# Performance work log

Hardware: AMD Instinct MI355X
Metric: run time of the kernel (lower is better)

## Reference

```python
import jax, jax.numpy as jnp
import numpy as np

G, P, D, K = 64, 1024, 64, 6  # graphs, nodes/graph, features, knn k
N = G * P


def _lin_init(k, shape):
    s = 1.0 / np.sqrt(shape[0])
    return jax.random.uniform(k, shape, minval=-s, maxval=s, dtype=jnp.float32)


def setup_inputs() -> dict:
    key = jax.random.key(0)
    ks = jax.random.split(key, 16)
    return {
        "x": jax.random.normal(ks[0], (N, D), jnp.float32),
        "batchidxs": jnp.repeat(jnp.arange(G, dtype=jnp.int32), P),
        "pre_W1": _lin_init(ks[1], (D, D)),
        "pre_b1": _lin_init(ks[2], (D,)),
        "pre_a1": jnp.full((D,), 0.25, jnp.float32),
        "pre_W2": _lin_init(ks[3], (D, D)),
        "pre_b2": _lin_init(ks[4], (D,)),
        "pre_a2": jnp.full((D,), 0.25, jnp.float32),
        "bn_gamma": jnp.ones((D,), jnp.float32),
        "bn_beta": jnp.zeros((D,), jnp.float32),
        "act_a": jnp.full((D,), 0.25, jnp.float32),
        "conv_W": jax.random.normal(ks[5], (4, D, D), jnp.float32) / np.sqrt(D),
        "conv_b": jnp.zeros((4, D), jnp.float32),
        "ffn_W1": _lin_init(ks[6], (5 * D, 5 * D)),
        "ffn_b1": _lin_init(ks[7], (5 * D,)),
        "ffn_W2": _lin_init(ks[8], (5 * D, 1)),
        "ffn_b2": _lin_init(ks[9], (1,)),
    }


def _prelu(x, a):
    return jnp.where(x >= 0, x, a * x)


def _knn_edges(x):
    """knn_graph with k=K per graph (equal-sized graphs). Returns (src, dst) global idx."""
    xg = x.reshape(G, P, D)

    def knn_one(pts):  # [P, D] -> [P, K] local neighbor idx
        sq = jnp.sum(pts * pts, axis=-1)
        d2 = sq[:, None] + sq[None, :] - 2.0 * (pts @ pts.T)
        d2 = d2 + jnp.eye(P, dtype=d2.dtype) * 1e10  # exclude self-loop
        _, idx = jax.lax.top_k(-d2, K)
        return idx

    nbr = jax.vmap(knn_one)(xg)  # [G, P, K]
    offs = (jnp.arange(G, dtype=nbr.dtype) * P)[:, None, None]
    src = (nbr + offs).reshape(-1)  # source (neighbor) nodes x_j
    dst = jnp.broadcast_to(jnp.arange(P, dtype=nbr.dtype)[None, :, None] + offs,
                           (G, P, K)).reshape(-1)  # target (query) nodes
    return src, dst


def reference(x, batchidxs, pre_W1, pre_b1, pre_a1, pre_W2, pre_b2, pre_a2,
              bn_gamma, bn_beta, act_a, conv_W, conv_b,
              ffn_W1, ffn_b1, ffn_W2, ffn_b2):
    src, dst = _knn_edges(x)

    # pre_nn: Linear -> PReLU -> Linear -> PReLU -> BatchNorm (training stats)
    h = _prelu(x @ pre_W1 + pre_b1, pre_a1)
    h = _prelu(h @ pre_W2 + pre_b2, pre_a2)
    mu = jnp.mean(h, axis=0)
    var = jnp.var(h, axis=0)
    h = (h - mu) * jax.lax.rsqrt(var + 1e-5) * bn_gamma + bn_beta

    xs = [h]
    for i in range(4):
        msg = h[src] @ conv_W[i] + conv_b[i]            # gather + transform [E, D]
        aggr = jax.ops.segment_sum(msg, dst, num_segments=N)  # scatter-add
        h = _prelu(aggr + h, act_a)                     # shared PReLU act
        xs.append(h)

    hc = jnp.concatenate(xs, axis=-1)                   # JumpingKnowledge 'cat' [N, 5D]
    pooled = jax.ops.segment_sum(hc, batchidxs, num_segments=G)  # global_add_pool [G, 5D]

    # hlv_dnn FFN(5D -> 1): Linear -> LeakyReLU -> Linear
    z = pooled @ ffn_W1 + ffn_b1
    z = jnp.where(z >= 0, z, 0.01 * z)
    return z @ ffn_W2 + ffn_b2
```

## Files before the change

### kernel.cpp

```cpp
#include <hip/hip_runtime.h>


typedef float4 f4;
typedef unsigned short ushort;
typedef unsigned int uint;
typedef _Float16 f16;
typedef _Float16 f16x8 __attribute__((ext_vector_type(8)));
typedef float f32x16 __attribute__((ext_vector_type(16)));

#define FMA16(sv, wv) do { \
  a0.x += (sv).x*(wv).x; a0.y += (sv).x*(wv).y; a0.z += (sv).x*(wv).z; a0.w += (sv).x*(wv).w; \
  a1.x += (sv).y*(wv).x; a1.y += (sv).y*(wv).y; a1.z += (sv).y*(wv).z; a1.w += (sv).y*(wv).w; \
  a2.x += (sv).z*(wv).x; a2.y += (sv).z*(wv).y; a2.z += (sv).z*(wv).z; a2.w += (sv).z*(wv).w; \
  a3.x += (sv).w*(wv).x; a3.y += (sv).w*(wv).y; a3.z += (sv).w*(wv).z; a3.w += (sv).w*(wv).w; \
} while (0)

union HU { f16 h; ushort u; };
__device__ __forceinline__ ushort f2h_u(float f) { HU x; x.h = (f16)f; return x.u; }
__device__ __forceinline__ f16 u2h(ushort u) { HU x; x.u = u; return x.h; }

__device__ __forceinline__ uint med3u(uint a, uint b, uint c) {
  uint d;
  asm("v_med3_u32 %0, %1, %2, %3" : "=v"(d) : "v"(a), "v"(b), "v"(c));
  return d;
}

#define INSM(x) do { \
  m5 = med3u((x), m4, m5); \
  m4 = med3u((x), m3, m4); \
  m3 = med3u((x), m2, m3); \
  m2 = med3u((x), m1, m2); \
  m1 = med3u((x), m0, m1); \
  m0 = max(m0, (x)); \
} while (0)

__global__ __launch_bounds__(256, 4) void kknn(const ushort* __restrict__ xf16,
                                               const uint* __restrict__ sq2,
                                               int* __restrict__ nbr) {
  __shared__ uint skey[4][32][6];
  const int tid = threadIdx.x;
  const int lane = tid & 63;
  const int w = tid >> 6;
  const int q = lane & 31;
  const int h = lane >> 5;
  const int g = blockIdx.x >> 5;
  const int qtile = blockIdx.x & 31;
  const int gbase = g << 10;
  const int qloc = qtile * 32 + q;
  const int qglob = gbase + qloc;

  f16x8 Q0, Q1, Q2, Q3;
  {
    const ushort* qp = xf16 + (size_t)qglob * 64 + 8 * h;
    Q0 = *(const f16x8*)(qp);       Q1 = *(const f16x8*)(qp + 16);
    Q2 = *(const f16x8*)(qp + 32);  Q3 = *(const f16x8*)(qp + 48);
  }
  f16x8 Bsq = {(f16)0, (f16)0, (f16)0, (f16)0, (f16)0, (f16)0, (f16)0, (f16)0};
  if (h == 0) { Bsq[0] = (f16)1.0f; Bsq[1] = (f16)1.0f; }

  uint m0 = 0, m1 = 0, m2 = 0, m3 = 0, m4 = 0, m5 = 0;

  for (int cc = 0; cc < 8; ++cc) {
    const int cg = w * 8 + cc;
    const int cb = gbase + cg * 32;
    const ushort* cp = xf16 + (size_t)(cb + q) * 64 + 8 * h;
    f16x8 A0 = *(const f16x8*)(cp);       f16x8 A1 = *(const f16x8*)(cp + 16);
    f16x8 A2 = *(const f16x8*)(cp + 32);  f16x8 A3 = *(const f16x8*)(cp + 48);
    uint sv = sq2[cb + q];
    f16x8 Asq = {(f16)0, (f16)0, (f16)0, (f16)0, (f16)0, (f16)0, (f16)0, (f16)0};
    if (h == 0) { Asq[0] = u2h((ushort)(sv & 0xffffu)); Asq[1] = u2h((ushort)(sv >> 16)); }

    f32x16 acc = {1536.f,1536.f,1536.f,1536.f,1536.f,1536.f,1536.f,1536.f,
                  1536.f,1536.f,1536.f,1536.f,1536.f,1536.f,1536.f,1536.f};
    acc = __builtin_amdgcn_mfma_f32_32x32x16_f16(A0, Q0, acc, 0, 0, 0);
    acc = __builtin_amdgcn_mfma_f32_32x32x16_f16(A1, Q1, acc, 0, 0, 0);
    acc = __builtin_amdgcn_mfma_f32_32x32x16_f16(A2, Q2, acc, 0, 0, 0);
    acc = __builtin_amdgcn_mfma_f32_32x32x16_f16(A3, Q3, acc, 0, 0, 0);
    acc = __builtin_amdgcn_mfma_f32_32x32x16_f16(Asq, Bsq, acc, 0, 0, 0);

    const int cl0 = cg * 32 + 4 * h;
    const uint kb = (uint)(1023 - cl0);
    if (cg == qtile) {
#pragma unroll
      for (int r = 0; r < 16; ++r) {
        const int pat = (r & 3) + 8 * (r >> 2);
        uint u = __float_as_uint(acc[r]);
        uint key = (((u << 9) & 0xFFFFFC00u) | kb) - (uint)pat;
        if (cl0 + pat == qloc) key = 0u;
        INSM(key);
      }
    } else {
#pragma unroll
      for (int r = 0; r < 16; ++r) {
        const int pat = (r & 3) + 8 * (r >> 2);
        uint u = __float_as_uint(acc[r]);
        uint key = (((u << 9) & 0xFFFFFC00u) | kb) - (uint)pat;
        INSM(key);
      }
    }
  }

  {
    uint p0 = (uint)__shfl_xor((int)m0, 32, 64);
    uint p1 = (uint)__shfl_xor((int)m1, 32, 64);
    uint p2 = (uint)__shfl_xor((int)m2, 32, 64);
    uint p3 = (uint)__shfl_xor((int)m3, 32, 64);
    uint p4 = (uint)__shfl_xor((int)m4, 32, 64);
    uint p5 = (uint)__shfl_xor((int)m5, 32, 64);
    INSM(p0); INSM(p1); INSM(p2); INSM(p3); INSM(p4); INSM(p5);
  }
  if (h == 0) {
    skey[w][q][0] = m0; skey[w][q][1] = m1; skey[w][q][2] = m2;
    skey[w][q][3] = m3; skey[w][q][4] = m4; skey[w][q][5] = m5;
  }
  __syncthreads();

  if (tid < 32) {
    uint m0 = skey[0][tid][0], m1 = skey[0][tid][1], m2 = skey[0][tid][2];
    uint m3 = skey[0][tid][3], m4 = skey[0][tid][4], m5 = skey[0][tid][5];
#pragma unroll
    for (int ww = 1; ww < 4; ++ww)
#pragma unroll
      for (int k = 0; k < 6; ++k)
        INSM(skey[ww][tid][k]);
    const int ob = (gbase + qtile * 32 + tid) * 6;
    nbr[ob + 0] = gbase + 1023 - (int)(m0 & 1023u);
    nbr[ob + 1] = gbase + 1023 - (int)(m1 & 1023u);
    nbr[ob + 2] = gbase + 1023 - (int)(m2 & 1023u);
    nbr[ob + 3] = gbase + 1023 - (int)(m3 & 1023u);
    nbr[ob + 4] = gbase + 1023 - (int)(m4 & 1023u);
    nbr[ob + 5] = gbase + 1023 - (int)(m5 & 1023u);
  }
}

__global__ __launch_bounds__(256) void kpre(const float* __restrict__ x,
    const float* __restrict__ W1, const float* __restrict__ b1, const float* __restrict__ p1,
    const float* __restrict__ W2, const float* __restrict__ b2, const float* __restrict__ p2,
    float* __restrict__ hpre, float* __restrict__ gsumg, float* __restrict__ gsq,
    ushort* __restrict__ xf16, uint* __restrict__ sq2) {
  __shared__ float xT[64][68];
  __shared__ float yT[64][68];
  __shared__ float W1l[64][64];
  __shared__ float W2l[64][64];
  __shared__ float bb1[64], aa1[64], bb2[64], aa2[64];
  __shared__ float ls[64], lq[64];
  __shared__ float ls2[64][4];
  const int tid = threadIdx.x;
  const int base = blockIdx.x * 64;
  const int g = base >> 10;
#pragma unroll
  for (int k = 0; k < 16; ++k) {
    int idx = tid + 256 * k;
    W1l[idx >> 6][idx & 63] = W1[idx];
    W2l[idx >> 6][idx & 63] = W2[idx];
  }
  if (tid < 64) {
    bb1[tid] = b1[tid]; aa1[tid] = p1[tid]; bb2[tid] = b2[tid]; aa2[tid] = p2[tid];
    ls[tid] = 0.f; lq[tid] = 0.f;
  }
  const int il = tid >> 2, qq = tid & 3;
  {
    const f4* src = (const f4*)(x + (size_t)(base + il) * 64) + qq * 4;
    float ssq = 0.f;
#pragma unroll
    for (int m = 0; m < 4; ++m) {
      f4 v = src[m];
      int d0 = qq * 16 + m * 4;
      xT[d0+0][il] = v.x; xT[d0+1][il] = v.y; xT[d0+2][il] = v.z; xT[d0+3][il] = v.w;
      ushort4 o4;
      o4.x = f2h_u(v.x); o4.y = f2h_u(v.y); o4.z = f2h_u(v.z); o4.w = f2h_u(v.w);
      *(ushort4*)(xf16 + (size_t)(base + il) * 64 + d0) = o4;
      ssq += v.x*v.x + v.y*v.y + v.z*v.z + v.w*v.w;
    }
    ls2[il][qq] = ssq;
  }
  __syncthreads();
  if (tid < 64) {
    float s = ls2[tid][0] + ls2[tid][1] + ls2[tid][2] + ls2[tid][3];
    float mm = -0.5f * s;
    ushort h1 = f2h_u(mm);
    HU t; t.u = h1;
    ushort h2 = f2h_u(mm - (float)t.h);
    sq2[base + tid] = (uint)h1 | ((uint)h2 << 16);
  }
  const int ti = tid & 15, to = tid >> 4;
  f4 a0 = {0.f,0.f,0.f,0.f}, a1 = a0, a2 = a0, a3 = a0;
#pragma unroll 16
  for (int d = 0; d < 64; ++d) {
    f4 sv = *(const f4*)&xT[d][4*ti];
    f4 wv = *(const f4*)&W1l[d][4*to];
    FMA16(sv, wv);
  }
#define EPI1(AR, r) { \
    const int row = 4*ti + (r); float v; \
    v = AR.x + bb1[4*to+0]; v = v >= 0.f ? v : aa1[4*to+0]*v; yT[4*to+0][row] = v; \
    v = AR.y + bb1[4*to+1]; v = v >= 0.f ? v : aa1[4*to+1]*v; yT[4*to+1][row] = v; \
    v = AR.z + bb1[4*to+2]; v = v >= 0.f ? v : aa1[4*to+2]*v; yT[4*to+2][row] = v; \
    v = AR.w + bb1[4*to+3]; v = v >= 0.f ? v : aa1[4*to+3]*v; yT[4*to+3][row] = v; }
  EPI1(a0, 0) EPI1(a1, 1) EPI1(a2, 2) EPI1(a3, 3)
#undef EPI1
  __syncthreads();
  a0.x=a0.y=a0.z=a0.w=0.f; a1=a0; a2=a0; a3=a0;
#pragma unroll 16
  for (int d = 0; d < 64; ++d) {
    f4 sv = *(const f4*)&yT[d][4*ti];
    f4 wv = *(const f4*)&W2l[d][4*to];
    FMA16(sv, wv);
  }
  float fs0=0.f,fs1=0.f,fs2=0.f,fs3=0.f, fq0=0.f,fq1=0.f,fq2=0.f,fq3=0.f;
#define EPI2(AR, r) { \
    const int i = base + 4*ti + (r); f4 ov; float v; \
    v = AR.x + bb2[4*to+0]; ov.x = v >= 0.f ? v : aa2[4*to+0]*v; \
    v = AR.y + bb2[4*to+1]; ov.y = v >= 0.f ? v : aa2[4*to+1]*v; \
    v = AR.z + bb2[4*to+2]; ov.z = v >= 0.f ? v : aa2[4*to+2]*v; \
    v = AR.w + bb2[4*to+3]; ov.w = v >= 0.f ? v : aa2[4*to+3]*v; \
    fs0 += ov.x; fq0 += ov.x*ov.x; fs1 += ov.y; fq1 += ov.y*ov.y; \
    fs2 += ov.z; fq2 += ov.z*ov.z; fs3 += ov.w; fq3 += ov.w*ov.w; \
    *((f4*)(hpre + (size_t)i * 64) + to) = ov; }
  EPI2(a0, 0) EPI2(a1, 1) EPI2(a2, 2) EPI2(a3, 3)
#undef EPI2
  atomicAdd(&ls[4*to+0], fs0); atomicAdd(&lq[4*to+0], fq0);
  atomicAdd(&ls[4*to+1], fs1); atomicAdd(&lq[4*to+1], fq1);
  atomicAdd(&ls[4*to+2], fs2); atomicAdd(&lq[4*to+2], fq2);
  atomicAdd(&ls[4*to+3], fs3); atomicAdd(&lq[4*to+3], fq3);
  __syncthreads();
  if (tid < 64) {
    atomicAdd(&gsumg[g * 64 + tid], ls[tid]);
    atomicAdd(&gsq[tid], lq[tid]);
  }
}

__global__ void kfin(const float* __restrict__ gsumg, const float* __restrict__ gsq,
                     const float* __restrict__ gamma, const float* __restrict__ beta,
                     float* __restrict__ scale, float* __restrict__ shift,
                     float* __restrict__ pooled) {
  const int g = blockIdx.x, f = threadIdx.x;
  float s = 0.f;
  for (int g2 = 0; g2 < 64; ++g2) s += gsumg[g2 * 64 + f];
  float mu = s * (1.f / 65536.f);
  float var = gsq[f] * (1.f / 65536.f) - mu * mu;
  float sc = gamma[f] * rsqrtf(var + 1e-5f);
  float sh = beta[f] - mu * sc;
  pooled[g * 320 + f] = sc * gsumg[g * 64 + f] + 1024.f * sh;
  if (g == 0) { scale[f] = sc; shift[f] = sh; }
}

template <int BN>
__global__ __launch_bounds__(256) void kconv(const float* __restrict__ hIn,
    float* __restrict__ hOut, const int* __restrict__ nbr,
    const float* __restrict__ W, const float* __restrict__ bias,
    const float* __restrict__ act, const float* __restrict__ scale,
    const float* __restrict__ shift, float* __restrict__ pooled, int stageoff) {
  __shared__ float sT[64][68];
  __shared__ float Wl[64][64];
  __shared__ float bb[64], aa[64], pool[64];
  __shared__ float scl[64], shl[64];
  const int tid = threadIdx.x;
  const int base = blockIdx.x * 64;
  const int g = base >> 10;
#pragma unroll
  for (int k = 0; k < 16; ++k) { int idx = tid + 256 * k; Wl[idx >> 6][idx & 63] = W[idx]; }
  if (tid < 64) {
    bb[tid] = bias[tid]; aa[tid] = act[tid]; pool[tid] = 0.f;
    if (BN) { scl[tid] = scale[tid]; shl[tid] = shift[tid]; }
  }

  const int il = tid >> 2, qq = tid & 3;
  {
    f4 acc0 = {0.f,0.f,0.f,0.f}, acc1 = acc0, acc2 = acc0, acc3 = acc0;
    const int i = base + il;
#pragma unroll
    for (int k = 0; k < 6; ++k) {
      int j = nbr[i * 6 + k];
      const f4* hj = (const f4*)(hIn + (size_t)j * 64) + qq * 4;
      f4 v0 = hj[0], v1 = hj[1], v2 = hj[2], v3 = hj[3];
      acc0.x += v0.x; acc0.y += v0.y; acc0.z += v0.z; acc0.w += v0.w;
      acc1.x += v1.x; acc1.y += v1.y; acc1.z += v1.z; acc1.w += v1.w;
      acc2.x += v2.x; acc2.y += v2.y; acc2.z += v2.z; acc2.w += v2.w;
      acc3.x += v3.x; acc3.y += v3.y; acc3.z += v3.z; acc3.w += v3.w;
    }
    const int d0 = qq * 16;
    sT[d0+ 0][il]=acc0.x; sT[d0+ 1][il]=acc0.y; sT[d0+ 2][il]=acc0.z; sT[d0+ 3][il]=acc0.w;
    sT[d0+ 4][il]=acc1.x; sT[d0+ 5][il]=acc1.y; sT[d0+ 6][il]=acc1.z; sT[d0+ 7][il]=acc1.w;
    sT[d0+ 8][il]=acc2.x; sT[d0+ 9][il]=acc2.y; sT[d0+10][il]=acc2.z; sT[d0+11][il]=acc2.w;
    sT[d0+12][il]=acc3.x; sT[d0+13][il]=acc3.y; sT[d0+14][il]=acc3.z; sT[d0+15][il]=acc3.w;
  }
  __syncthreads();

  const int ti = tid & 15, to = tid >> 4;
  f4 a0 = {0.f,0.f,0.f,0.f}, a1 = a0, a2 = a0, a3 = a0;
  if (BN) {
#pragma unroll 16
    for (int d = 0; d < 64; ++d) {
      const float scd = scl[d], shd6 = 6.f * shl[d];
      f4 sv = *(const f4*)&sT[d][4*ti];
      sv.x = sv.x * scd + shd6; sv.y = sv.y * scd + shd6;
      sv.z = sv.z * scd + shd6; sv.w = sv.w * scd + shd6;
      f4 wv = *(const f4*)&Wl[d][4*to];
      FMA16(sv, wv);
    }
  } else {
#pragma unroll 16
    for (int d = 0; d < 64; ++d) {
      f4 sv = *(const f4*)&sT[d][4*ti];
      f4 wv = *(const f4*)&Wl[d][4*to];
      FMA16(sv, wv);
    }
  }

  const float bs0 = 6.f*bb[4*to+0], bs1 = 6.f*bb[4*to+1], bs2 = 6.f*bb[4*to+2], bs3 = 6.f*bb[4*to+3];
  const float av0 = aa[4*to+0], av1 = aa[4*to+1], av2 = aa[4*to+2], av3 = aa[4*to+3];
  const float rs0 = BN ? scl[4*to+0] : 1.f, rs1 = BN ? scl[4*to+1] : 1.f;
  const float rs2 = BN ? scl[4*to+2] : 1.f, rs3 = BN ? scl[4*to+3] : 1.f;
  const float rh0 = BN ? shl[4*to+0] : 0.f, rh1 = BN ? shl[4*to+1] : 0.f;
  const float rh2 = BN ? shl[4*to+2] : 0.f, rh3 = BN ? shl[4*to+3] : 0.f;
  float p0 = 0.f, pp1 = 0.f, pp2 = 0.f, pp3 = 0.f;
#define CEPI(AR, r) { \
    const int i = base + 4*ti + (r); \
    f4 res = *((const f4*)(hIn + (size_t)i * 64) + to); \
    f4 ov; float v; \
    v = AR.x + bs0 + res.x*rs0 + rh0; v = v >= 0.f ? v : av0 * v; ov.x = v; p0  += v; \
    v = AR.y + bs1 + res.y*rs1 + rh1; v = v >= 0.f ? v : av1 * v; ov.y = v; pp1 += v; \
    v = AR.z + bs2 + res.z*rs2 + rh2; v = v >= 0.f ? v : av2 * v; ov.z = v; pp2 += v; \
    v = AR.w + bs3 + res.w*rs3 + rh3; v = v >= 0.f ? v : av3 * v; ov.w = v; pp3 += v; \
    *((f4*)(hOut + (size_t)i * 64) + to) = ov; }
  CEPI(a0, 0) CEPI(a1, 1) CEPI(a2, 2) CEPI(a3, 3)
#undef CEPI
  atomicAdd(&pool[4*to+0], p0);
  atomicAdd(&pool[4*to+1], pp1);
  atomicAdd(&pool[4*to+2], pp2);
  atomicAdd(&pool[4*to+3], pp3);
  __syncthreads();
  if (tid < 64) atomicAdd(&pooled[g * 320 + stageoff + tid], pool[tid]);
}

__global__ __launch_bounds__(256) void kffn(const float* __restrict__ pooled,
    const float* __restrict__ W1, const float* __restrict__ b1,
    const float* __restrict__ W2, const float* __restrict__ b2,
    float* __restrict__ out) {
  __shared__ float pg[320];
  __shared__ float z1[320];
  __shared__ float red[4];
  const int g = blockIdx.x, tid = threadIdx.x;
  for (int i = tid; i < 320; i += 256) pg[i] = pooled[g * 320 + i];
  __syncthreads();
  for (int o = tid; o < 320; o += 256) {
    float acc = b1[o];
    for (int d = 0; d < 320; ++d) acc += pg[d] * W1[d * 320 + o];
    z1[o] = acc >= 0.f ? acc : 0.01f * acc;
  }
  __syncthreads();
  float p = 0.f;
  for (int o = tid; o < 320; o += 256) p += z1[o] * W2[o];
#pragma unroll
  for (int m = 32; m; m >>= 1) p += __shfl_xor(p, m, 64);
  if ((tid & 63) == 0) red[tid >> 6] = p;
  __syncthreads();
  if (tid == 0) out[g] = red[0] + red[1] + red[2] + red[3] + b2[0];
}

extern "C" void kernel_launch(void* const* d_in, const int* in_sizes, int n_in,
                              void* d_out, int out_size, void* d_ws, size_t ws_size,
                              hipStream_t stream) {
  const float* x        = (const float*)d_in[0];
  const float* pre_W1   = (const float*)d_in[2];
  const float* pre_b1   = (const float*)d_in[3];
  const float* pre_a1   = (const float*)d_in[4];
  const float* pre_W2   = (const float*)d_in[5];
  const float* pre_b2   = (const float*)d_in[6];
  const float* pre_a2   = (const float*)d_in[7];
  const float* bn_gamma = (const float*)d_in[8];
  const float* bn_beta  = (const float*)d_in[9];
  const float* act_a    = (const float*)d_in[10];
  const float* conv_W   = (const float*)d_in[11];
  const float* conv_b   = (const float*)d_in[12];
  const float* ffn_W1   = (const float*)d_in[13];
  const float* ffn_b1   = (const float*)d_in[14];
  const float* ffn_W2   = (const float*)d_in[15];
  const float* ffn_b2   = (const float*)d_in[16];
  float* out = (float*)d_out;

  float* ws = (float*)d_ws;
  float* hA = ws;
  float* hB = ws + 4194304;
  ushort* xf16 = (ushort*)hB;
  uint*   sq2  = (uint*)(hB + 2097152);
  int*   nbr   = (int*)(ws + 8388608);
  float* stats = ws + 8388608 + 393216;
  float* gsq    = stats;
  float* gsumg  = stats + 64;
  float* scale  = stats + 64 + 4096;
  float* shift  = stats + 64 + 4096 + 64;
  float* pooled = stats + 64 + 4096 + 128;

  hipMemsetAsync(stats, 0, (64 + 4096 + 128 + 64 * 320) * sizeof(float), stream);

  kpre  <<<1024, 256, 0, stream>>>(x, pre_W1, pre_b1, pre_a1, pre_W2, pre_b2, pre_a2,
                                   hA, gsumg, gsq, xf16, sq2);
  kknn  <<<2048, 256, 0, stream>>>(xf16, sq2, nbr);
  kfin  <<<64, 64, 0, stream>>>(gsumg, gsq, bn_gamma, bn_beta, scale, shift, pooled);
  kconv<1><<<1024, 256, 0, stream>>>(hA, hB, nbr, conv_W,         conv_b,       act_a, scale, shift, pooled, 64);
  kconv<0><<<1024, 256, 0, stream>>>(hB, hA, nbr, conv_W + 4096,  conv_b + 64,  act_a, scale, shift, pooled, 128);
  kconv<0><<<1024, 256, 0, stream>>>(hA, hB, nbr, conv_W + 8192,  conv_b + 128, act_a, scale, shift, pooled, 192);
  kconv<0><<<1024, 256, 0, stream>>>(hB, hA, nbr, conv_W + 12288, conv_b + 192, act_a, scale, shift, pooled, 256);
  kffn  <<<64, 256, 0, stream>>>(pooled, ffn_W1, ffn_b1, ffn_W2, ffn_b2, out);
}
```

Baseline: 300.9 us.

## Use fp16 MFMA for pre-MLP and conv layers with fp16 activations

```diff
diff --git a/kernel.cpp b/kernel.cpp
--- a/kernel.cpp
+++ b/kernel.cpp
@@ -8,12 +8,7 @@
 typedef _Float16 f16x8 __attribute__((ext_vector_type(8)));
 typedef float f32x16 __attribute__((ext_vector_type(16)));
 
-#define FMA16(sv, wv) do { \
-  a0.x += (sv).x*(wv).x; a0.y += (sv).x*(wv).y; a0.z += (sv).x*(wv).z; a0.w += (sv).x*(wv).w; \
-  a1.x += (sv).y*(wv).x; a1.y += (sv).y*(wv).y; a1.z += (sv).y*(wv).z; a1.w += (sv).y*(wv).w; \
-  a2.x += (sv).z*(wv).x; a2.y += (sv).z*(wv).y; a2.z += (sv).z*(wv).z; a2.w += (sv).z*(wv).w; \
-  a3.x += (sv).w*(wv).x; a3.y += (sv).w*(wv).y; a3.z += (sv).w*(wv).z; a3.w += (sv).w*(wv).w; \
-} while (0)
+#define Z16 {0.f,0.f,0.f,0.f,0.f,0.f,0.f,0.f,0.f,0.f,0.f,0.f,0.f,0.f,0.f,0.f}
 
 union HU { f16 h; ushort u; };
 __device__ __forceinline__ ushort f2h_u(float f) { HU x; x.h = (f16)f; return x.u; }
@@ -33,6 +28,17 @@
   m1 = med3u((x), m0, m1); \
   m0 = max(m0, (x)); \
 } while (0)
+
+__global__ void kwprep(const float* __restrict__ W1, const float* __restrict__ W2,
+                       const float* __restrict__ convW, ushort* __restrict__ wt) {
+  const int m = blockIdx.x;
+  const float* src = (m == 0) ? W1 : (m == 1) ? W2 : convW + (m - 2) * 4096;
+  ushort* dst = wt + m * 4096;
+  for (int i = threadIdx.x; i < 4096; i += 256) {
+    int k = i >> 6, n = i & 63;
+    dst[n * 64 + k] = f2h_u(src[i]);
+  }
+}
 
 __global__ __launch_bounds__(256, 4) void kknn(const ushort* __restrict__ xf16,
                                                const uint* __restrict__ sq2,
@@ -133,96 +139,105 @@
   }
 }
 
-__global__ __launch_bounds__(256) void kpre(const float* __restrict__ x,
-    const float* __restrict__ W1, const float* __restrict__ b1, const float* __restrict__ p1,
-    const float* __restrict__ W2, const float* __restrict__ b2, const float* __restrict__ p2,
-    float* __restrict__ hpre, float* __restrict__ gsumg, float* __restrict__ gsq,
+__global__ __launch_bounds__(256) void kpre(
+    const float* __restrict__ x, const ushort* __restrict__ w1t,
+    const float* __restrict__ b1, const float* __restrict__ p1,
+    const ushort* __restrict__ w2t, const float* __restrict__ b2,
+    const float* __restrict__ p2, ushort* __restrict__ hout,
+    float* __restrict__ gsumg, float* __restrict__ gsq,
     ushort* __restrict__ xf16, uint* __restrict__ sq2) {
-  __shared__ float xT[64][68];
-  __shared__ float yT[64][68];
-  __shared__ float W1l[64][64];
-  __shared__ float W2l[64][64];
-  __shared__ float bb1[64], aa1[64], bb2[64], aa2[64];
+  __shared__ ushort tile[4][32][72];
   __shared__ float ls[64], lq[64];
-  __shared__ float ls2[64][4];
-  const int tid = threadIdx.x;
-  const int base = blockIdx.x * 64;
-  const int g = base >> 10;
-#pragma unroll
-  for (int k = 0; k < 16; ++k) {
-    int idx = tid + 256 * k;
-    W1l[idx >> 6][idx & 63] = W1[idx];
-    W2l[idx >> 6][idx & 63] = W2[idx];
-  }
-  if (tid < 64) {
-    bb1[tid] = b1[tid]; aa1[tid] = p1[tid]; bb2[tid] = b2[tid]; aa2[tid] = p2[tid];
-    ls[tid] = 0.f; lq[tid] = 0.f;
-  }
-  const int il = tid >> 2, qq = tid & 3;
+  const int tid = threadIdx.x, lane = tid & 63, w = tid >> 6;
+  const int q = lane & 31, h = lane >> 5;
+  const int rbase = blockIdx.x * 128 + w * 32;
+  const int row = rbase + q;
+  const int g = blockIdx.x >> 3;
+  if (tid < 64) { ls[tid] = 0.f; lq[tid] = 0.f; }
+  __syncthreads();
+
+  f16x8 Ax[4]; float ssq = 0.f;
+  const float* xp = x + (size_t)row * 64 + 8 * h;
+  ushort* xo = xf16 + (size_t)row * 64 + 8 * h;
+#pragma unroll
+  for (int ks = 0; ks < 4; ++ks) {
+    f4 a = *(const f4*)(xp + 16 * ks);
+    f4 b = *(const f4*)(xp + 16 * ks + 4);
+    f16x8 f;
+    f[0] = (f16)a.x; f[1] = (f16)a.y; f[2] = (f16)a.z; f[3] = (f16)a.w;
+    f[4] = (f16)b.x; f[5] = (f16)b.y; f[6] = (f16)b.z; f[7] = (f16)b.w;
+    Ax[ks] = f;
+    *(f16x8*)(xo + 16 * ks) = f;
+    ssq += a.x*a.x + a.y*a.y + a.z*a.z + a.w*a.w + b.x*b.x + b.y*b.y + b.z*b.z + b.w*b.w;
+  }
+  ssq += __shfl_xor(ssq, 32, 64);
+  if (h == 0) {
+    float mm = -0.5f * ssq;
+    ushort u1 = f2h_u(mm); HU t1; t1.u = u1;
+    ushort u2 = f2h_u(mm - (float)t1.h);
+    sq2[row] = (uint)u1 | ((uint)u2 << 16);
+  }
+
+  f32x16 c0 = Z16, c1 = Z16;
+#pragma unroll
+  for (int ks = 0; ks < 4; ++ks) {
+    f16x8 B0 = *(const f16x8*)(w1t + q * 64 + 16 * ks + 8 * h);
+    f16x8 B1 = *(const f16x8*)(w1t + (q + 32) * 64 + 16 * ks + 8 * h);
+    c0 = __builtin_amdgcn_mfma_f32_32x32x16_f16(Ax[ks], B0, c0, 0, 0, 0);
+    c1 = __builtin_amdgcn_mfma_f32_32x32x16_f16(Ax[ks], B1, c1, 0, 0, 0);
+  }
   {
-    const f4* src = (const f4*)(x + (size_t)(base + il) * 64) + qq * 4;
-    float ssq = 0.f;
-#pragma unroll
-    for (int m = 0; m < 4; ++m) {
-      f4 v = src[m];
-      int d0 = qq * 16 + m * 4;
-      xT[d0+0][il] = v.x; xT[d0+1][il] = v.y; xT[d0+2][il] = v.z; xT[d0+3][il] = v.w;
-      ushort4 o4;
-      o4.x = f2h_u(v.x); o4.y = f2h_u(v.y); o4.z = f2h_u(v.z); o4.w = f2h_u(v.w);
-      *(ushort4*)(xf16 + (size_t)(base + il) * 64 + d0) = o4;
-      ssq += v.x*v.x + v.y*v.y + v.z*v.z + v.w*v.w;
-    }
-    ls2[il][qq] = ssq;
-  }
-  __syncthreads();
-  if (tid < 64) {
-    float s = ls2[tid][0] + ls2[tid][1] + ls2[tid][2] + ls2[tid][3];
-    float mm = -0.5f * s;
-    ushort h1 = f2h_u(mm);
-    HU t; t.u = h1;
-    ushort h2 = f2h_u(mm - (float)t.h);
-    sq2[base + tid] = (uint)h1 | ((uint)h2 << 16);
-  }
-  const int ti = tid & 15, to = tid >> 4;
-  f4 a0 = {0.f,0.f,0.f,0.f}, a1 = a0, a2 = a0, a3 = a0;
-#pragma unroll 16
-  for (int d = 0; d < 64; ++d) {
-    f4 sv = *(const f4*)&xT[d][4*ti];
-    f4 wv = *(const f4*)&W1l[d][4*to];
-    FMA16(sv, wv);
-  }
-#define EPI1(AR, r) { \
-    const int row = 4*ti + (r); float v; \
-    v = AR.x + bb1[4*to+0]; v = v >= 0.f ? v : aa1[4*to+0]*v; yT[4*to+0][row] = v; \
-    v = AR.y + bb1[4*to+1]; v = v >= 0.f ? v : aa1[4*to+1]*v; yT[4*to+1][row] = v; \
-    v = AR.z + bb1[4*to+2]; v = v >= 0.f ? v : aa1[4*to+2]*v; yT[4*to+2][row] = v; \
-    v = AR.w + bb1[4*to+3]; v = v >= 0.f ? v : aa1[4*to+3]*v; yT[4*to+3][row] = v; }
-  EPI1(a0, 0) EPI1(a1, 1) EPI1(a2, 2) EPI1(a3, 3)
-#undef EPI1
-  __syncthreads();
-  a0.x=a0.y=a0.z=a0.w=0.f; a1=a0; a2=a0; a3=a0;
-#pragma unroll 16
-  for (int d = 0; d < 64; ++d) {
-    f4 sv = *(const f4*)&yT[d][4*ti];
-    f4 wv = *(const f4*)&W2l[d][4*to];
-    FMA16(sv, wv);
-  }
-  float fs0=0.f,fs1=0.f,fs2=0.f,fs3=0.f, fq0=0.f,fq1=0.f,fq2=0.f,fq3=0.f;
-#define EPI2(AR, r) { \
-    const int i = base + 4*ti + (r); f4 ov; float v; \
-    v = AR.x + bb2[4*to+0]; ov.x = v >= 0.f ? v : aa2[4*to+0]*v; \
-    v = AR.y + bb2[4*to+1]; ov.y = v >= 0.f ? v : aa2[4*to+1]*v; \
-    v = AR.z + bb2[4*to+2]; ov.z = v >= 0.f ? v : aa2[4*to+2]*v; \
-    v = AR.w + bb2[4*to+3]; ov.w = v >= 0.f ? v : aa2[4*to+3]*v; \
-    fs0 += ov.x; fq0 += ov.x*ov.x; fs1 += ov.y; fq1 += ov.y*ov.y; \
-    fs2 += ov.z; fq2 += ov.z*ov.z; fs3 += ov.w; fq3 += ov.w*ov.w; \
-    *((f4*)(hpre + (size_t)i * 64) + to) = ov; }
-  EPI2(a0, 0) EPI2(a1, 1) EPI2(a2, 2) EPI2(a3, 3)
-#undef EPI2
-  atomicAdd(&ls[4*to+0], fs0); atomicAdd(&lq[4*to+0], fq0);
-  atomicAdd(&ls[4*to+1], fs1); atomicAdd(&lq[4*to+1], fq1);
-  atomicAdd(&ls[4*to+2], fs2); atomicAdd(&lq[4*to+2], fq2);
-  atomicAdd(&ls[4*to+3], fs3); atomicAdd(&lq[4*to+3], fq3);
+    const float bb0 = b1[q], aa0 = p1[q], bb1 = b1[q + 32], aa1 = p1[q + 32];
+#pragma unroll
+    for (int r = 0; r < 16; ++r) {
+      const int nd = (r & 3) + 8 * (r >> 2) + 4 * h;
+      float v0 = c0[r] + bb0; v0 = v0 >= 0.f ? v0 : aa0 * v0;
+      float v1 = c1[r] + bb1; v1 = v1 >= 0.f ? v1 : aa1 * v1;
+      tile[w][nd][q] = f2h_u(v0);
+      tile[w][nd][q + 32] = f2h_u(v1);
+    }
+  }
+  f16x8 Ah[4];
+#pragma unroll
+  for (int ks = 0; ks < 4; ++ks)
+    Ah[ks] = *(const f16x8*)&tile[w][q][16 * ks + 8 * h];
+
+  f32x16 d0 = Z16, d1 = Z16;
+#pragma unroll
+  for (int ks = 0; ks < 4; ++ks) {
+    f16x8 B0 = *(const f16x8*)(w2t + q * 64 + 16 * ks + 8 * h);
+    f16x8 B1 = *(const f16x8*)(w2t + (q + 32) * 64 + 16 * ks + 8 * h);
+    d0 = __builtin_amdgcn_mfma_f32_32x32x16_f16(Ah[ks], B0, d0, 0, 0, 0);
+    d1 = __builtin_amdgcn_mfma_f32_32x32x16_f16(Ah[ks], B1, d1, 0, 0, 0);
+  }
+  {
+    const float bb0 = b2[q], aa0 = p2[q], bb1 = b2[q + 32], aa1 = p2[q + 32];
+    float s0 = 0.f, q0 = 0.f, s1 = 0.f, q1 = 0.f;
+#pragma unroll
+    for (int r = 0; r < 16; ++r) {
+      const int nd = (r & 3) + 8 * (r >> 2) + 4 * h;
+      float v0 = d0[r] + bb0; v0 = v0 >= 0.f ? v0 : aa0 * v0;
+      float v1 = d1[r] + bb1; v1 = v1 >= 0.f ? v1 : aa1 * v1;
+      ushort u0 = f2h_u(v0), u1 = f2h_u(v1);
+      HU t0, t1; t0.u = u0; t1.u = u1;
+      float r0 = (float)t0.h, r1 = (float)t1.h;
+      s0 += r0; q0 += r0 * r0; s1 += r1; q1 += r1 * r1;
+      tile[w][nd][q] = u0;
+      tile[w][nd][q + 32] = u1;
+    }
+    s0 += __shfl_xor(s0, 32, 64); q0 += __shfl_xor(q0, 32, 64);
+    s1 += __shfl_xor(s1, 32, 64); q1 += __shfl_xor(q1, 32, 64);
+    if (h == 0) {
+      atomicAdd(&ls[q], s0); atomicAdd(&lq[q], q0);
+      atomicAdd(&ls[q + 32], s1); atomicAdd(&lq[q + 32], q1);
+    }
+  }
+  ushort* ho = hout + (size_t)row * 64 + 8 * h;
+#pragma unroll
+  for (int ks = 0; ks < 4; ++ks) {
+    f16x8 v = *(const f16x8*)&tile[w][q][16 * ks + 8 * h];
+    *(f16x8*)(ho + 16 * ks) = v;
+  }
   __syncthreads();
   if (tid < 64) {
     atomicAdd(&gsumg[g * 64 + tid], ls[tid]);
@@ -246,90 +261,113 @@
 }
 
 template <int BN>
-__global__ __launch_bounds__(256) void kconv(const float* __restrict__ hIn,
-    float* __restrict__ hOut, const int* __restrict__ nbr,
-    const float* __restrict__ W, const float* __restrict__ bias,
-    const float* __restrict__ act, const float* __restrict__ scale,
-    const float* __restrict__ shift, float* __restrict__ pooled, int stageoff) {
-  __shared__ float sT[64][68];
-  __shared__ float Wl[64][64];
-  __shared__ float bb[64], aa[64], pool[64];
-  __shared__ float scl[64], shl[64];
-  const int tid = threadIdx.x;
-  const int base = blockIdx.x * 64;
-  const int g = base >> 10;
-#pragma unroll
-  for (int k = 0; k < 16; ++k) { int idx = tid + 256 * k; Wl[idx >> 6][idx & 63] = W[idx]; }
-  if (tid < 64) {
-    bb[tid] = bias[tid]; aa[tid] = act[tid]; pool[tid] = 0.f;
-    if (BN) { scl[tid] = scale[tid]; shl[tid] = shift[tid]; }
-  }
-
-  const int il = tid >> 2, qq = tid & 3;
+__global__ __launch_bounds__(256) void kconv(
+    const ushort* __restrict__ hIn, ushort* __restrict__ hOut,
+    const int* __restrict__ nbr, const ushort* __restrict__ wt,
+    const float* __restrict__ bias, const float* __restrict__ act,
+    const float* __restrict__ scale, const float* __restrict__ shift,
+    float* __restrict__ pooled, int stageoff) {
+  __shared__ ushort tile[4][32][72];
+  __shared__ float pool[64];
+  const int tid = threadIdx.x, lane = tid & 63, w = tid >> 6;
+  const int q = lane & 31, h = lane >> 5;
+  const int nbase = blockIdx.x * 128 + w * 32;
+  const int node = nbase + q;
+  const int g = blockIdx.x >> 3;
+  if (tid < 64) pool[tid] = 0.f;
+  __syncthreads();
+
+  const int* np = nbr + (size_t)node * 6;
+  const int j0 = np[0], j1 = np[1], j2 = np[2], j3 = np[3], j4 = np[4], j5 = np[5];
+
+  f16x8 Af[4];
+#pragma unroll
+  for (int ks = 0; ks < 4; ++ks) {
+    const int off = 16 * ks + 8 * h;
+    float s0=0.f,s1=0.f,s2=0.f,s3=0.f,s4=0.f,s5=0.f,s6=0.f,s7=0.f;
+#define ACC6(J) { f16x8 v = *(const f16x8*)(hIn + (size_t)(J) * 64 + off); \
+    s0 += (float)v[0]; s1 += (float)v[1]; s2 += (float)v[2]; s3 += (float)v[3]; \
+    s4 += (float)v[4]; s5 += (float)v[5]; s6 += (float)v[6]; s7 += (float)v[7]; }
+    ACC6(j0) ACC6(j1) ACC6(j2) ACC6(j3) ACC6(j4) ACC6(j5)
+#undef ACC6
+    if (BN) {
+      f4 sa = *(const f4*)(scale + off), sb = *(const f4*)(scale + off + 4);
+      f4 ha = *(const f4*)(shift + off), hb = *(const f4*)(shift + off + 4);
+      s0 = s0*sa.x + 6.f*ha.x; s1 = s1*sa.y + 6.f*ha.y;
+      s2 = s2*sa.z + 6.f*ha.z; s3 = s3*sa.w + 6.f*ha.w;
+      s4 = s4*sb.x + 6.f*hb.x; s5 = s5*sb.y + 6.f*hb.y;
+      s6 = s6*sb.z + 6.f*hb.z; s7 = s7*sb.w + 6.f*hb.w;
+    }
+    f16x8 f;
+    f[0]=(f16)s0; f[1]=(f16)s1; f[2]=(f16)s2; f[3]=(f16)s3;
+    f[4]=(f16)s4; f[5]=(f16)s5; f[6]=(f16)s6; f[7]=(f16)s7;
+    Af[ks] = f;
+  }
+
+  f32x16 c0 = Z16, c1 = Z16;
+#pragma unroll
+  for (int ks = 0; ks < 4; ++ks) {
+    f16x8 B0 = *(const f16x8*)(wt + q * 64 + 16 * ks + 8 * h);
+    f16x8 B1 = *(const f16x8*)(wt + (q + 32) * 64 + 16 * ks + 8 * h);
+    c0 = __builtin_amdgcn_mfma_f32_32x32x16_f16(Af[ks], B0, c0, 0, 0, 0);
+    c1 = __builtin_amdgcn_mfma_f32_32x32x16_f16(Af[ks], B1, c1, 0, 0, 0);
+  }
   {
-    f4 acc0 = {0.f,0.f,0.f,0.f}, acc1 = acc0, acc2 = acc0, acc3 = acc0;
-    const int i = base + il;
-#pragma unroll
-    for (int k = 0; k < 6; ++k) {
-      int j = nbr[i * 6 + k];
-      const f4* hj = (const f4*)(hIn + (size_t)j * 64) + qq * 4;
-      f4 v0 = hj[0], v1 = hj[1], v2 = hj[2], v3 = hj[3];
-      acc0.x += v0.x; acc0.y += v0.y; acc0.z += v0.z; acc0.w += v0.w;
-      acc1.x += v1.x; acc1.y += v1.y; acc1.z += v1.z; acc1.w += v1.w;
-      acc2.x += v2.x; acc2.y += v2.y; acc2.z += v2.z; acc2.w += v2.w;
-      acc3.x += v3.x; acc3.y += v3.y; acc3.z += v3.z; acc3.w += v3.w;
-    }
-    const int d0 = qq * 16;
-    sT[d0+ 0][il]=acc0.x; sT[d0+ 1][il]=acc0.y; sT[d0+ 2][il]=acc0.z; sT[d0+ 3][il]=acc0.w;
-    sT[d0+ 4][il]=acc1.x; sT[d0+ 5][il]=acc1.y; sT[d0+ 6][il]=acc1.z; sT[d0+ 7][il]=acc1.w;
-    sT[d0+ 8][il]=acc2.x; sT[d0+ 9][il]=acc2.y; sT[d0+10][il]=acc2.z; sT[d0+11][il]=acc2.w;
-    sT[d0+12][il]=acc3.x; sT[d0+13][il]=acc3.y; sT[d0+14][il]=acc3.z; sT[d0+15][il]=acc3.w;
-  }
-  __syncthreads();
-
-  const int ti = tid & 15, to = tid >> 4;
-  f4 a0 = {0.f,0.f,0.f,0.f}, a1 = a0, a2 = a0, a3 = a0;
+    const float bb0 = 6.f * bias[q], bb1 = 6.f * bias[q + 32];
+#pragma unroll
+    for (int r = 0; r < 16; ++r) {
+      const int nd = (r & 3) + 8 * (r >> 2) + 4 * h;
+      tile[w][nd][q] = f2h_u(c0[r] + bb0);
+      tile[w][nd][q + 32] = f2h_u(c1[r] + bb1);
+    }
+  }
+
+  const int a = lane >> 3, b = lane & 7;
+  f4 aa0 = *(const f4*)(act + 8 * b), aa1 = *(const f4*)(act + 8 * b + 4);
+  f4 rs0, rs1, rh0, rh1;
   if (BN) {
-#pragma unroll 16
-    for (int d = 0; d < 64; ++d) {
-      const float scd = scl[d], shd6 = 6.f * shl[d];
-      f4 sv = *(const f4*)&sT[d][4*ti];
-      sv.x = sv.x * scd + shd6; sv.y = sv.y * scd + shd6;
-      sv.z = sv.z * scd + shd6; sv.w = sv.w * scd + shd6;
-      f4 wv = *(const f4*)&Wl[d][4*to];
-      FMA16(sv, wv);
-    }
-  } else {
-#pragma unroll 16
-    for (int d = 0; d < 64; ++d) {
-      f4 sv = *(const f4*)&sT[d][4*ti];
-      f4 wv = *(const f4*)&Wl[d][4*to];
-      FMA16(sv, wv);
-    }
-  }
-
-  const float bs0 = 6.f*bb[4*to+0], bs1 = 6.f*bb[4*to+1], bs2 = 6.f*bb[4*to+2], bs3 = 6.f*bb[4*to+3];
-  const float av0 = aa[4*to+0], av1 = aa[4*to+1], av2 = aa[4*to+2], av3 = aa[4*to+3];
-  const float rs0 = BN ? scl[4*to+0] : 1.f, rs1 = BN ? scl[4*to+1] : 1.f;
-  const float rs2 = BN ? scl[4*to+2] : 1.f, rs3 = BN ? scl[4*to+3] : 1.f;
-  const float rh0 = BN ? shl[4*to+0] : 0.f, rh1 = BN ? shl[4*to+1] : 0.f;
-  const float rh2 = BN ? shl[4*to+2] : 0.f, rh3 = BN ? shl[4*to+3] : 0.f;
-  float p0 = 0.f, pp1 = 0.f, pp2 = 0.f, pp3 = 0.f;
-#define CEPI(AR, r) { \
-    const int i = base + 4*ti + (r); \
-    f4 res = *((const f4*)(hIn + (size_t)i * 64) + to); \
-    f4 ov; float v; \
-    v = AR.x + bs0 + res.x*rs0 + rh0; v = v >= 0.f ? v : av0 * v; ov.x = v; p0  += v; \
-    v = AR.y + bs1 + res.y*rs1 + rh1; v = v >= 0.f ? v : av1 * v; ov.y = v; pp1 += v; \
-    v = AR.z + bs2 + res.z*rs2 + rh2; v = v >= 0.f ? v : av2 * v; ov.z = v; pp2 += v; \
-    v = AR.w + bs3 + res.w*rs3 + rh3; v = v >= 0.f ? v : av3 * v; ov.w = v; pp3 += v; \
-    *((f4*)(hOut + (size_t)i * 64) + to) = ov; }
-  CEPI(a0, 0) CEPI(a1, 1) CEPI(a2, 2) CEPI(a3, 3)
-#undef CEPI
-  atomicAdd(&pool[4*to+0], p0);
-  atomicAdd(&pool[4*to+1], pp1);
-  atomicAdd(&pool[4*to+2], pp2);
-  atomicAdd(&pool[4*to+3], pp3);
+    rs0 = *(const f4*)(scale + 8 * b); rs1 = *(const f4*)(scale + 8 * b + 4);
+    rh0 = *(const f4*)(shift + 8 * b); rh1 = *(const f4*)(shift + 8 * b + 4);
+  }
+  f4 ps0 = {0.f,0.f,0.f,0.f}, ps1 = ps0;
+#pragma unroll
+  for (int r = 0; r < 4; ++r) {
+    const int nd = 4 * a + r;
+    const size_t gn = (size_t)(nbase + nd) * 64 + 8 * b;
+    f16x8 z = *(const f16x8*)&tile[w][nd][8 * b];
+    f16x8 ro = *(const f16x8*)(hIn + gn);
+    float v0 = (float)z[0] + (BN ? rs0.x * (float)ro[0] + rh0.x : (float)ro[0]);
+    float v1 = (float)z[1] + (BN ? rs0.y * (float)ro[1] + rh0.y : (float)ro[1]);
+    float v2 = (float)z[2] + (BN ? rs0.z * (float)ro[2] + rh0.z : (float)ro[2]);
+    float v3 = (float)z[3] + (BN ? rs0.w * (float)ro[3] + rh0.w : (float)ro[3]);
+    float v4 = (float)z[4] + (BN ? rs1.x * (float)ro[4] + rh1.x : (float)ro[4]);
+    float v5 = (float)z[5] + (BN ? rs1.y * (float)ro[5] + rh1.y : (float)ro[5]);
+    float v6 = (float)z[6] + (BN ? rs1.z * (float)ro[6] + rh1.z : (float)ro[6]);
+    float v7 = (float)z[7] + (BN ? rs1.w * (float)ro[7] + rh1.w : (float)ro[7]);
+    v0 = v0 >= 0.f ? v0 : aa0.x * v0;  v1 = v1 >= 0.f ? v1 : aa0.y * v1;
+    v2 = v2 >= 0.f ? v2 : aa0.z * v2;  v3 = v3 >= 0.f ? v3 : aa0.w * v3;
+    v4 = v4 >= 0.f ? v4 : aa1.x * v4;  v5 = v5 >= 0.f ? v5 : aa1.y * v5;
+    v6 = v6 >= 0.f ? v6 : aa1.z * v6;  v7 = v7 >= 0.f ? v7 : aa1.w * v7;
+    ps0.x += v0; ps0.y += v1; ps0.z += v2; ps0.w += v3;
+    ps1.x += v4; ps1.y += v5; ps1.z += v6; ps1.w += v7;
+    f16x8 o;
+    o[0]=(f16)v0; o[1]=(f16)v1; o[2]=(f16)v2; o[3]=(f16)v3;
+    o[4]=(f16)v4; o[5]=(f16)v5; o[6]=(f16)v6; o[7]=(f16)v7;
+    *(f16x8*)(hOut + gn) = o;
+  }
+#pragma unroll
+  for (int m = 8; m <= 32; m <<= 1) {
+    ps0.x += __shfl_xor(ps0.x, m, 64); ps0.y += __shfl_xor(ps0.y, m, 64);
+    ps0.z += __shfl_xor(ps0.z, m, 64); ps0.w += __shfl_xor(ps0.w, m, 64);
+    ps1.x += __shfl_xor(ps1.x, m, 64); ps1.y += __shfl_xor(ps1.y, m, 64);
+    ps1.z += __shfl_xor(ps1.z, m, 64); ps1.w += __shfl_xor(ps1.w, m, 64);
+  }
+  if (a == 0) {
+    atomicAdd(&pool[8 * b + 0], ps0.x); atomicAdd(&pool[8 * b + 1], ps0.y);
+    atomicAdd(&pool[8 * b + 2], ps0.z); atomicAdd(&pool[8 * b + 3], ps0.w);
+    atomicAdd(&pool[8 * b + 4], ps1.x); atomicAdd(&pool[8 * b + 5], ps1.y);
+    atomicAdd(&pool[8 * b + 6], ps1.z); atomicAdd(&pool[8 * b + 7], ps1.w);
+  }
   __syncthreads();
   if (tid < 64) atomicAdd(&pooled[g * 320 + stageoff + tid], pool[tid]);
 }
@@ -380,13 +418,13 @@
   const float* ffn_b2   = (const float*)d_in[16];
   float* out = (float*)d_out;
 
-  float* ws = (float*)d_ws;
-  float* hA = ws;
-  float* hB = ws + 4194304;
-  ushort* xf16 = (ushort*)hB;
-  uint*   sq2  = (uint*)(hB + 2097152);
-  int*   nbr   = (int*)(ws + 8388608);
-  float* stats = ws + 8388608 + 393216;
+  ushort* hA16 = (ushort*)d_ws;
+  ushort* hB16 = hA16 + 4194304;
+  ushort* xf16 = hB16 + 4194304;
+  uint*   sq2  = (uint*)(xf16 + 4194304);
+  int*    nbr  = (int*)(sq2 + 65536);
+  ushort* wt   = (ushort*)(nbr + 393216);
+  float* stats = (float*)(wt + 24576);
   float* gsq    = stats;
   float* gsumg  = stats + 64;
   float* scale  = stats + 64 + 4096;
@@ -395,13 +433,14 @@
 
   hipMemsetAsync(stats, 0, (64 + 4096 + 128 + 64 * 320) * sizeof(float), stream);
 
-  kpre  <<<1024, 256, 0, stream>>>(x, pre_W1, pre_b1, pre_a1, pre_W2, pre_b2, pre_a2,
-                                   hA, gsumg, gsq, xf16, sq2);
+  kwprep<<<6, 256, 0, stream>>>(pre_W1, pre_W2, conv_W, wt);
+  kpre  <<<512, 256, 0, stream>>>(x, wt, pre_b1, pre_a1, wt + 4096, pre_b2, pre_a2,
+                                  hA16, gsumg, gsq, xf16, sq2);
   kknn  <<<2048, 256, 0, stream>>>(xf16, sq2, nbr);
   kfin  <<<64, 64, 0, stream>>>(gsumg, gsq, bn_gamma, bn_beta, scale, shift, pooled);
-  kconv<1><<<1024, 256, 0, stream>>>(hA, hB, nbr, conv_W,         conv_b,       act_a, scale, shift, pooled, 64);
-  kconv<0><<<1024, 256, 0, stream>>>(hB, hA, nbr, conv_W + 4096,  conv_b + 64,  act_a, scale, shift, pooled, 128);
-  kconv<0><<<1024, 256, 0, stream>>>(hA, hB, nbr, conv_W + 8192,  conv_b + 128, act_a, scale, shift, pooled, 192);
-  kconv<0><<<1024, 256, 0, stream>>>(hB, hA, nbr, conv_W + 12288, conv_b + 192, act_a, scale, shift, pooled, 256);
+  kconv<1><<<512, 256, 0, stream>>>(hA16, hB16, nbr, wt + 2*4096, conv_b,       act_a, scale, shift, pooled, 64);
+  kconv<0><<<512, 256, 0, stream>>>(hB16, hA16, nbr, wt + 3*4096, conv_b + 64,  act_a, scale, shift, pooled, 128);
+  kconv<0><<<512, 256, 0, stream>>>(hA16, hB16, nbr, wt + 4*4096, conv_b + 128, act_a, scale, shift, pooled, 192);
+  kconv<0><<<512, 256, 0, stream>>>(hB16, hA16, nbr, wt + 5*4096, conv_b + 192, act_a, scale, shift, pooled, 256);
   kffn  <<<64, 256, 0, stream>>>(pooled, ffn_W1, ffn_b1, ffn_W2, ffn_b2, out);
 }
```

Measured after the change: 244.7 us. 1.23x faster.
